# Performance work log

Hardware: AMD Instinct MI355X
Metric: run time of the kernel (lower is better)

Reference implementation:

```python
import jax, jax.numpy as jnp
import numpy as np

DIM = 512; NH = 8; AG = 144; WIN = 18; PS = 12; B = 128; N0 = 320


def _pool_matrix(in_size, out_size):
    # PyTorch AdaptiveAvgPool2d window rule: start=floor(i*in/out), end=ceil((i+1)*in/out)
    P = np.zeros((out_size, in_size), np.float32)
    for i in range(out_size):
        s = (i * in_size) // out_size
        e = -((-(i + 1) * in_size) // out_size)
        P[i, s:e] = 1.0 / (e - s)
    return jnp.asarray(P)


def setup_inputs() -> dict:
    key = jax.random.key(0)
    ks = jax.random.split(key, 12)
    std = 0.02
    return {
        "x": jax.random.normal(ks[0], (B, N0, DIM), jnp.float32),
        "qkv_w": jax.random.normal(ks[1], (DIM, 3 * DIM), jnp.float32) * 0.02,
        "proj_w": jax.random.normal(ks[2], (DIM, DIM), jnp.float32) * 0.02,
        "proj_b": jnp.zeros((DIM,), jnp.float32),
        "dwc_w": jax.random.normal(ks[3], (DIM, 1, 3, 3), jnp.float32) * 0.1,
        "dwc_b": jnp.zeros((DIM,), jnp.float32),
        "an_bias": jax.random.normal(ks[4], (NH, AG, 7, 7), jnp.float32) * std,
        "na_bias": jax.random.normal(ks[5], (NH, AG, 7, 7), jnp.float32) * std,
        "ah_bias": jax.random.normal(ks[6], (1, NH, AG, WIN, 1), jnp.float32) * std,
        "aw_bias": jax.random.normal(ks[7], (1, NH, AG, 1, WIN), jnp.float32) * std,
        "ha_bias": jax.random.normal(ks[8], (1, NH, WIN, 1, AG), jnp.float32) * std,
        "wa_bias": jax.random.normal(ks[9], (1, NH, 1, WIN, AG), jnp.float32) * std,
    }


def reference(x, qkv_w, proj_w, proj_b, dwc_w, dwc_b,
              an_bias, na_bias, ah_bias, aw_bias, ha_bias, wa_bias):
    b, n0, c = x.shape
    x1 = jnp.pad(x, ((0, 0), (2, 2), (0, 0)))          # pad 2 tokens each side
    n = n0 + 4
    h = w = int(n ** 0.5)
    hd = c // NH
    scale = hd ** -0.5

    qkv = x1 @ qkv_w                                    # (b, n, 3c), no bias
    q, k, v = jnp.split(qkv, 3, axis=-1)

    # agent tokens: adaptive avg pool of q on the (h, w) grid to (PS, PS)
    P = _pool_matrix(h, PS)                             # (12, 18)
    qg = q.reshape(b, h, w, c)
    agent = jnp.einsum('oh,bhwc,pw->bopc', P, qg, P).reshape(b, AG, c)

    def heads(t):
        return t.reshape(b, n, NH, hd).transpose(0, 2, 1, 3)
    q, k, v = heads(q), heads(k), heads(v)              # (b, H, n, hd)
    ag = agent.reshape(b, AG, NH, hd).transpose(0, 2, 1, 3)  # (b, H, A, hd)

    # stage 1: agent <- keys  (ac_bias is concatenated then sliced off => no-op)
    pb1 = jax.image.resize(an_bias, (NH, AG, WIN, WIN), 'bilinear').reshape(1, NH, AG, WIN * WIN)
    pb2 = (ah_bias + aw_bias).reshape(1, NH, AG, WIN * WIN)
    agent_attn = jax.nn.softmax(
        jnp.einsum('bhad,bhnd->bhan', ag * scale, k) + pb1 + pb2, axis=-1)
    agent_v = jnp.einsum('bhan,bhnd->bhad', agent_attn, v)   # (b, H, A, hd)

    # stage 2: queries <- agents (ca_bias sliced off => no-op)
    ab1 = jax.image.resize(na_bias, (NH, AG, WIN, WIN), 'bilinear') \
        .reshape(1, NH, AG, WIN * WIN).transpose(0, 1, 3, 2)  # (1, H, n, A)
    ab2 = (ha_bias + wa_bias).reshape(1, NH, WIN * WIN, AG)
    q_attn = jax.nn.softmax(
        jnp.einsum('bhnd,bhad->bhna', q * scale, ag) + ab1 + ab2, axis=-1)
    out = jnp.einsum('bhna,bhad->bhnd', q_attn, agent_v)
    out = out.transpose(0, 2, 1, 3).reshape(b, n, c)

    # depthwise conv skip on v
    vimg = v.transpose(0, 2, 1, 3).reshape(b, h, w, c).transpose(0, 3, 1, 2)  # (b, c, h, w)
    dwc = jax.lax.conv_general_dilated(vimg, dwc_w, (1, 1), 'SAME',
                                       feature_group_count=c)
    dwc = dwc + dwc_b[None, :, None, None]
    out = out + dwc.transpose(0, 2, 3, 1).reshape(b, n, c)

    out = out @ proj_w + proj_b
    return out[:, 2:-2, :]
```

## Files before the change

### kernel.cpp

```cpp
#include <hip/hip_runtime.h>

typedef unsigned short u16;
typedef short bf16x8 __attribute__((ext_vector_type(8)));
typedef float f32x4 __attribute__((ext_vector_type(4)));

#define B_    128
#define N0_   320
#define C_    512
#define NH_   8
#define HD_   64
#define NTOK  324
#define H_    18
#define AG_   144
#define SCALE 0.125f

typedef __attribute__((address_space(3))) unsigned int as3_u32;
typedef __attribute__((address_space(1))) const unsigned int as1_u32;

__device__ __forceinline__ void gl_lds16(const void* g, void* l) {
  __builtin_amdgcn_global_load_lds((as1_u32*)(unsigned long long)g,
                                   (as3_u32*)(unsigned int)(unsigned long long)l,
                                   16, 0, 0);
}

__device__ __forceinline__ float bfu2f(u16 u) {
  union { unsigned int u; float f; } v; v.u = ((unsigned int)u) << 16; return v.f;
}
__device__ __forceinline__ u16 f2bfu(float f) {
  union { float f; unsigned int u; } v; v.f = f;
  unsigned int r = v.u + 0x7fffu + ((v.u >> 16) & 1u);
  return (u16)(r >> 16);
}

__global__ __launch_bounds__(256) void conv_x(const float* __restrict__ x, u16* __restrict__ xp)
{
  const int idx = blockIdx.x * 256 + threadIdx.x;
  const int row = idx >> 6, c8 = idx & 63;
  const int b = row / NTOK, t = row - b * NTOK;
  u16 o[8];
  if (t < 2 || t >= 322) {
    #pragma unroll
    for (int j = 0; j < 8; ++j) o[j] = 0;
  } else {
    const float* src = x + ((size_t)(b * N0_ + (t - 2))) * C_ + c8 * 8;
    const float4 f0 = *(const float4*)(src);
    const float4 f1 = *(const float4*)(src + 4);
    o[0]=f2bfu(f0.x); o[1]=f2bfu(f0.y); o[2]=f2bfu(f0.z); o[3]=f2bfu(f0.w);
    o[4]=f2bfu(f1.x); o[5]=f2bfu(f1.y); o[6]=f2bfu(f1.z); o[7]=f2bfu(f1.w);
  }
  *(bf16x8*)&xp[(size_t)row * C_ + c8 * 8] = *(bf16x8*)o;
}

__global__ __launch_bounds__(256) void tconv(const float* __restrict__ W, u16* __restrict__ Wt, int ncols)
{
  __shared__ float T[64][65];
  const int k0 = blockIdx.x * 64, n0 = blockIdx.y * 64;
  const int tid = threadIdx.x;
  const int rr = tid >> 4, cc = tid & 15;
  #pragma unroll
  for (int i = 0; i < 4; ++i) {
    const float4 f = *(const float4*)&W[(size_t)(k0 + i * 16 + rr) * ncols + n0 + cc * 4];
    T[i * 16 + rr][cc * 4 + 0] = f.x; T[i * 16 + rr][cc * 4 + 1] = f.y;
    T[i * 16 + rr][cc * 4 + 2] = f.z; T[i * 16 + rr][cc * 4 + 3] = f.w;
  }
  __syncthreads();
  #pragma unroll
  for (int i = 0; i < 4; ++i) {
    const int n = i * 16 + rr;
    ushort4 u;
    u.x = f2bfu(T[cc * 4 + 0][n]); u.y = f2bfu(T[cc * 4 + 1][n]);
    u.z = f2bfu(T[cc * 4 + 2][n]); u.w = f2bfu(T[cc * 4 + 3][n]);
    *(ushort4*)&Wt[(size_t)(n0 + n) * 512 + k0 + cc * 4] = u;
  }
}

template<int MODE>
__global__ __launch_bounds__(256) void mfma_gemm(
    const u16* __restrict__ A, const u16* __restrict__ Bt,
    u16* __restrict__ qb, u16* __restrict__ kb, u16* __restrict__ vb,
    const float* __restrict__ bias, float* __restrict__ outf)
{
  __shared__ __align__(16) u16 As[128 * 64];
  __shared__ __align__(16) u16 Bs[128 * 64];
  const int bx = blockIdx.x;
  const int by = blockIdx.y;
  const int tid = threadIdx.x;
  const int wv = tid >> 6, lane = tid & 63;
  const int lr = lane & 15, lk = lane >> 4;
  const int wr = wv >> 1, wc = wv & 1;
  const int si = lane >> 3, slot = lane & 7;

  size_t arow_src[4];
  #pragma unroll
  for (int jj = 0; jj < 4; ++jj) {
    const int rl = (wv * 4 + jj) * 8 + si;
    const int r = by * 128 + rl;
    if (MODE == 0) {
      arow_src[jj] = (size_t)r * 512;
    } else {
      const int b2 = r / N0_, ii = r - b2 * N0_;
      arow_src[jj] = ((size_t)b2 * 8 * NTOK + (ii + 2)) * 64;
    }
  }

  f32x4 acc[4][4] = {};
  for (int k0 = 0; k0 < 512; k0 += 64) {
    __syncthreads();
    #pragma unroll
    for (int jj = 0; jj < 4; ++jj) {
      const int rl = (wv * 4 + jj) * 8 + si;
      const int c = slot ^ (rl & 7);
      const u16* asrc = (MODE == 0)
          ? (A + arow_src[jj] + k0 + c * 8)
          : (A + arow_src[jj] + (size_t)(k0 >> 6) * (NTOK * 64) + c * 8);
      gl_lds16(asrc, (char*)As + (wv * 4 + jj) * 1024);
      gl_lds16(Bt + (size_t)(bx * 128 + rl) * 512 + k0 + c * 8,
               (char*)Bs + (wv * 4 + jj) * 1024);
    }
    __syncthreads();
    #pragma unroll
    for (int kk = 0; kk < 2; ++kk) {
      bf16x8 af[4], bf[4];
      #pragma unroll
      for (int m = 0; m < 4; ++m) {
        const int row = wr * 64 + m * 16 + lr;
        af[m] = *(const bf16x8*)((const char*)As + row * 128 + (((kk * 4 + lk) ^ (row & 7)) << 4));
      }
      #pragma unroll
      for (int n = 0; n < 4; ++n) {
        const int row = wc * 64 + n * 16 + lr;
        bf[n] = *(const bf16x8*)((const char*)Bs + row * 128 + (((kk * 4 + lk) ^ (row & 7)) << 4));
      }
      #pragma unroll
      for (int m = 0; m < 4; ++m)
        #pragma unroll
        for (int n = 0; n < 4; ++n)
          acc[m][n] = __builtin_amdgcn_mfma_f32_16x16x32_bf16(bf[n], af[m], acc[m][n], 0, 0, 0);
    }
  }

  if (MODE == 0) {
    const int mat = (bx * 128) >> 9;
    u16* outp = (mat == 0) ? qb : (mat == 1) ? kb : vb;
    #pragma unroll
    for (int m = 0; m < 4; ++m) {
      const int row = by * 128 + wr * 64 + m * 16 + lr;
      const int b = row / NTOK, t = row - b * NTOK;
      #pragma unroll
      for (int n = 0; n < 4; ++n) {
        const int col = bx * 128 + wc * 64 + n * 16 + lk * 4;
        const int rem = col & 511, h = rem >> 6, d = rem & 63;
        ushort4 u;
        u.x = f2bfu(acc[m][n][0]); u.y = f2bfu(acc[m][n][1]);
        u.z = f2bfu(acc[m][n][2]); u.w = f2bfu(acc[m][n][3]);
        *(ushort4*)&outp[(((size_t)(b * NH_ + h)) * NTOK + t) * HD_ + d] = u;
      }
    }
  } else {
    #pragma unroll
    for (int m = 0; m < 4; ++m) {
      const int row = by * 128 + wr * 64 + m * 16 + lr;
      #pragma unroll
      for (int n = 0; n < 4; ++n) {
        const int col = bx * 128 + wc * 64 + n * 16 + lk * 4;
        float4 o;
        o.x = acc[m][n][0] + bias[col + 0];
        o.y = acc[m][n][1] + bias[col + 1];
        o.z = acc[m][n][2] + bias[col + 2];
        o.w = acc[m][n][3] + bias[col + 3];
        *(float4*)&outf[(size_t)row * C_ + col] = o;
      }
    }
  }
}

__global__ void bias_kernel(const float* __restrict__ an, const float* __restrict__ na,
                            const float* __restrict__ ah, const float* __restrict__ aw,
                            const float* __restrict__ ha, const float* __restrict__ wa,
                            u16* __restrict__ bANT, u16* __restrict__ bNAT)
{
  const int blk = blockIdx.x;
  const int h = blk / AG_, a = blk - h * AG_;
  const int tid = threadIdx.x;
  if (tid >= NTOK) return;
  const int y = tid / H_, x = tid - y * H_;
  float cy = (y + 0.5f) * (7.0f / 18.0f) - 0.5f; cy = fminf(fmaxf(cy, 0.f), 6.f);
  float cx = (x + 0.5f) * (7.0f / 18.0f) - 0.5f; cx = fminf(fmaxf(cx, 0.f), 6.f);
  const int y0 = (int)floorf(cy); const float ty = cy - y0; const int y1 = min(y0 + 1, 6);
  const int x0 = (int)floorf(cx); const float tx = cx - x0; const int x1 = min(x0 + 1, 6);
  const float w00 = (1.f - ty) * (1.f - tx), w01 = (1.f - ty) * tx;
  const float w10 = ty * (1.f - tx), w11 = ty * tx;
  const float* anp = an + (size_t)blk * 49;
  const float* nap = na + (size_t)blk * 49;
  const float van = w00 * anp[y0*7+x0] + w01 * anp[y0*7+x1] + w10 * anp[y1*7+x0] + w11 * anp[y1*7+x1];
  const float vna = w00 * nap[y0*7+x0] + w01 * nap[y0*7+x1] + w10 * nap[y1*7+x0] + w11 * nap[y1*7+x1];
  bANT[((size_t)h * NTOK + tid) * AG_ + a] =
      f2bfu(van + ah[(size_t)blk * H_ + y] + aw[(size_t)blk * H_ + x]);
  bNAT[((size_t)h * AG_ + a) * NTOK + tid] =
      f2bfu(vna + ha[((size_t)h * H_ + y) * AG_ + a] + wa[((size_t)h * H_ + x) * AG_ + a]);
}

__global__ __launch_bounds__(512) void pool_kernel(const u16* __restrict__ qb, u16* __restrict__ agb)
{
  const int blk = blockIdx.x;
  const int b = blk / AG_, a = blk - b * AG_;
  const int o = a / 12, pc = a - o * 12;
  const int y0 = (3 * o) >> 1, x0 = (3 * pc) >> 1;
  const int c = threadIdx.x; const int h = c >> 6, d = c & 63;
  const size_t base = ((size_t)(b * NH_ + h)) * NTOK * HD_ + d;
  const int t00 = (y0 * H_ + x0) * HD_;
  const float v = bfu2f(qb[base + t00]) + bfu2f(qb[base + t00 + HD_])
                + bfu2f(qb[base + t00 + H_ * HD_]) + bfu2f(qb[base + t00 + H_ * HD_ + HD_]);
  agb[((size_t)(b * NH_ + h)) * AG_ * HD_ + a * HD_ + d] = f2bfu(0.25f * v);
}

__global__ __launch_bounds__(512) void dwc_kernel(
    const u16* __restrict__ vb, const float* __restrict__ dwc_w,
    const float* __restrict__ dwc_b, u16* __restrict__ aob)
{
  __shared__ __align__(16) u16 vL[NTOK * 64];
  const int hb = blockIdx.x, h = hb >> 7, b = hb & 127;
  const int bh = b * NH_ + h;
  const int tid = threadIdx.x;
  const bf16x8* vs = (const bf16x8*)(vb + (size_t)bh * NTOK * HD_);
  for (int idx = tid; idx < NTOK * 8; idx += 512)
    ((bf16x8*)vL)[idx] = vs[idx];
  const int d = tid & 63, tg = tid >> 6;
  float w9[9];
  #pragma unroll
  for (int j = 0; j < 9; ++j) w9[j] = dwc_w[(size_t)(h * 64 + d) * 9 + j];
  const float cb = dwc_b[h * 64 + d];
  __syncthreads();
  u16* aout = aob + (size_t)bh * NTOK * HD_;
  for (int t = tg; t < NTOK; t += 8) {
    const int y = t / H_, x = t - y * H_;
    float conv = cb;
    #pragma unroll
    for (int ky = 0; ky < 3; ++ky) {
      const int yy = y + ky - 1;
      if (yy < 0 || yy >= H_) continue;
      #pragma unroll
      for (int kx = 0; kx < 3; ++kx) {
        const int xc = x + kx - 1;
        if (xc < 0 || xc >= H_) continue;
        conv += w9[ky * 3 + kx] * bfu2f(vL[(yy * H_ + xc) * 64 + d]);
      }
    }
    aout[(size_t)t * HD_ + d] = f2bfu(conv);
  }
}

__global__ __launch_bounds__(576) void stage1_k(
    const u16* __restrict__ kb, const u16* __restrict__ vb,
    const u16* __restrict__ agb, const u16* __restrict__ bANT,
    u16* __restrict__ avbT)
{
  __shared__ __align__(16) u16 vT[64 * 360];
  __shared__ __align__(16) u16 pW[9][16][40];
  const int hb = blockIdx.x, h = hb & 7, bbase = (hb >> 3) * 2;
  const int tid = threadIdx.x;
  const int mt = tid >> 6, l = tid & 63, lr = l & 15, lk = l >> 4;

  for (int bb2 = 0; bb2 < 2; ++bb2) {
    const int bh = (bbase + bb2) * NH_ + h;

    const u16* vsrc = vb + (size_t)bh * NTOK * HD_;
    for (int idx = tid; idx < 64 * 45; idx += 576) {
      const int d = idx & 63, c = idx >> 6;
      bf16x8 tv;
      #pragma unroll
      for (int j = 0; j < 8; ++j) {
        const int n = c * 8 + j;
        tv[j] = (n < NTOK) ? (short)vsrc[(size_t)n * HD_ + d] : (short)0;
      }
      *(bf16x8*)&vT[d * 360 + c * 8] = tv;
    }

    const u16* aga = agb + ((size_t)bh * AG_ + mt * 16 + lr) * HD_ + lk * 8;
    const bf16x8 a0 = *(const bf16x8*)(aga);
    const bf16x8 a1 = *(const bf16x8*)(aga + 32);

    f32x4 acc[21];
    const u16* kbase = kb + (size_t)bh * NTOK * HD_ + lk * 8;
    __builtin_amdgcn_s_setprio(1);
    #pragma unroll
    for (int nt = 0; nt < 21; ++nt) {
      const bf16x8 b0 = *(const bf16x8*)(kbase + (size_t)(nt * 16 + lr) * HD_);
      const bf16x8 b1 = *(const bf16x8*)(kbase + (size_t)(nt * 16 + lr) * HD_ + 32);
      f32x4 c = {0.f, 0.f, 0.f, 0.f};
      c = __builtin_amdgcn_mfma_f32_16x16x32_bf16(a0, b0, c, 0, 0, 0);
      c = __builtin_amdgcn_mfma_f32_16x16x32_bf16(a1, b1, c, 0, 0, 0);
      acc[nt] = c;
    }
    __builtin_amdgcn_s_setprio(0);

    float mx[4] = {-1e30f, -1e30f, -1e30f, -1e30f};
    #pragma unroll
    for (int nt = 0; nt < 21; ++nt) {
      const int t = nt * 16 + lr;
      const bool valid = (nt < 20) || (lr < 4);
      ushort4 b4 = make_ushort4(0, 0, 0, 0);
      if (valid)
        b4 = *(const ushort4*)&bANT[((size_t)h * NTOK + t) * AG_ + mt * 16 + lk * 4];
      #pragma unroll
      for (int r = 0; r < 4; ++r) {
        float s = -1e30f;
        if (valid) s = acc[nt][r] * SCALE + bfu2f(((const u16*)&b4)[r]);
        acc[nt][r] = s;
        mx[r] = fmaxf(mx[r], s);
      }
    }
    #pragma unroll
    for (int r = 0; r < 4; ++r) {
      #pragma unroll
      for (int o = 1; o < 16; o <<= 1) mx[r] = fmaxf(mx[r], __shfl_xor(mx[r], o));
    }
    float sm[4] = {0.f, 0.f, 0.f, 0.f};
    #pragma unroll
    for (int nt = 0; nt < 21; ++nt) {
      #pragma unroll
      for (int r = 0; r < 4; ++r) {
        const float e = __expf(acc[nt][r] - mx[r]);
        acc[nt][r] = e;
        sm[r] += e;
      }
    }
    #pragma unroll
    for (int r = 0; r < 4; ++r) {
      #pragma unroll
      for (int o = 1; o < 16; o <<= 1) sm[r] += __shfl_xor(sm[r], o);
      sm[r] = 1.0f / sm[r];
    }

    __syncthreads();

    f32x4 ov[4];
    #pragma unroll
    for (int nt2 = 0; nt2 < 4; ++nt2) ov[nt2] = (f32x4){0.f, 0.f, 0.f, 0.f};
    for (int ks = 0; ks < 11; ++ks) {
      #pragma unroll
      for (int half = 0; half < 2; ++half) {
        const int nt = 2 * ks + half;
        #pragma unroll
        for (int r = 0; r < 4; ++r)
          pW[mt][lk * 4 + r][half * 16 + lr] = (nt < 21) ? f2bfu(acc[nt][r] * sm[r]) : (u16)0;
      }
      const bf16x8 pa = *(const bf16x8*)&pW[mt][lr][lk * 8];
      __builtin_amdgcn_s_setprio(1);
      #pragma unroll
      for (int nt2 = 0; nt2 < 4; ++nt2) {
        const bf16x8 vf = *(const bf16x8*)&vT[(nt2 * 16 + lr) * 360 + ks * 32 + lk * 8];
        ov[nt2] = __builtin_amdgcn_mfma_f32_16x16x32_bf16(pa, vf, ov[nt2], 0, 0, 0);
      }
      __builtin_amdgcn_s_setprio(0);
    }

    __syncthreads();

    u16* avTL = vT;
    #pragma unroll
    for (int nt2 = 0; nt2 < 4; ++nt2) {
      ushort4 u;
      u.x = f2bfu(ov[nt2][0]); u.y = f2bfu(ov[nt2][1]);
      u.z = f2bfu(ov[nt2][2]); u.w = f2bfu(ov[nt2][3]);
      *(ushort4*)&avTL[(nt2 * 16 + lr) * 168 + mt * 16 + lk * 4] = u;
    }
    for (int idx = tid; idx < 128; idx += 576)
      *(bf16x8*)&avTL[(idx >> 1) * 168 + 144 + (idx & 1) * 8] = (bf16x8){0,0,0,0,0,0,0,0};

    __syncthreads();

    u16* dst = avbT + (size_t)bh * 64 * 160;
    for (int idx = tid; idx < 64 * 20; idx += 576) {
      const int d = idx / 20, c = idx - d * 20;
      *(bf16x8*)&dst[d * 160 + c * 8] = *(const bf16x8*)&avTL[d * 168 + c * 8];
    }
    __syncthreads();
  }
}

__global__ __launch_bounds__(512, 6) void stage2_k(
    const u16* __restrict__ qb, const u16* __restrict__ agb,
    const u16* __restrict__ avbT, const u16* __restrict__ bNAT,
    u16* __restrict__ aob)
{
  __shared__ __align__(16) u16 avT[64 * 168];
  __shared__ __align__(16) u16 pW[8][16][40];
  __shared__ __align__(16) u16 oB[8][16][72];
  const int hb = blockIdx.x, h = hb & 7, bbase = (hb >> 3) * 2;
  const int tid = threadIdx.x;
  const int wv = tid >> 6, l = tid & 63, lr = l & 15, lk = l >> 4;

  for (int bb2 = 0; bb2 < 2; ++bb2) {
    const int bh = (bbase + bb2) * NH_ + h;

    const u16* src = avbT + (size_t)bh * 64 * 160;
    for (int idx = tid; idx < 64 * 20; idx += 512) {
      const int d = idx / 20, c = idx - d * 20;
      *(bf16x8*)&avT[d * 168 + c * 8] = *(const bf16x8*)&src[d * 160 + c * 8];
    }
    __syncthreads();

    u16* aout = aob + (size_t)bh * NTOK * HD_;
    for (int mt2 = wv; mt2 < 21; mt2 += 8) {
      const int arow = min(mt2 * 16 + lr, NTOK - 1);
      const u16* qa = qb + ((size_t)bh * NTOK + arow) * HD_ + lk * 8;
      const bf16x8 qa0 = *(const bf16x8*)(qa);
      const bf16x8 qa1 = *(const bf16x8*)(qa + 32);

      f32x4 acc2[9];
      __builtin_amdgcn_s_setprio(1);
      #pragma unroll
      for (int nt = 0; nt < 9; ++nt) {
        const u16* bp = agb + ((size_t)bh * AG_ + nt * 16 + lr) * HD_ + lk * 8;
        f32x4 c = {0.f, 0.f, 0.f, 0.f};
        c = __builtin_amdgcn_mfma_f32_16x16x32_bf16(qa0, *(const bf16x8*)(bp), c, 0, 0, 0);
        c = __builtin_amdgcn_mfma_f32_16x16x32_bf16(qa1, *(const bf16x8*)(bp + 32), c, 0, 0, 0);
        acc2[nt] = c;
      }
      __builtin_amdgcn_s_setprio(0);

      float mx2[4] = {-1e30f, -1e30f, -1e30f, -1e30f};
      const int t0 = mt2 * 16 + lk * 4;
      #pragma unroll
      for (int nt = 0; nt < 9; ++nt) {
        const ushort4 b4 = *(const ushort4*)&bNAT[((size_t)h * AG_ + nt * 16 + lr) * NTOK + t0];
        #pragma unroll
        for (int r = 0; r < 4; ++r) {
          const float s = acc2[nt][r] * SCALE + bfu2f(((const u16*)&b4)[r]);
          acc2[nt][r] = s;
          mx2[r] = fmaxf(mx2[r], s);
        }
      }
      #pragma unroll
      for (int r = 0; r < 4; ++r) {
        #pragma unroll
        for (int o = 1; o < 16; o <<= 1) mx2[r] = fmaxf(mx2[r], __shfl_xor(mx2[r], o));
      }
      float sm2[4] = {0.f, 0.f, 0.f, 0.f};
      #pragma unroll
      for (int nt = 0; nt < 9; ++nt) {
        #pragma unroll
        for (int r = 0; r < 4; ++r) {
          const float e = __expf(acc2[nt][r] - mx2[r]);
          acc2[nt][r] = e;
          sm2[r] += e;
        }
      }
      #pragma unroll
      for (int r = 0; r < 4; ++r) {
        #pragma unroll
        for (int o = 1; o < 16; o <<= 1) sm2[r] += __shfl_xor(sm2[r], o);
        sm2[r] = 1.0f / sm2[r];
      }

      f32x4 ov2[4];
      #pragma unroll
      for (int dt = 0; dt < 4; ++dt) ov2[dt] = (f32x4){0.f, 0.f, 0.f, 0.f};
      for (int ks = 0; ks < 5; ++ks) {
        #pragma unroll
        for (int half = 0; half < 2; ++half) {
          const int nt = 2 * ks + half;
          #pragma unroll
          for (int r = 0; r < 4; ++r)
            pW[wv][lk * 4 + r][half * 16 + lr] = (nt < 9) ? f2bfu(acc2[nt][r] * sm2[r]) : (u16)0;
        }
        const bf16x8 pa = *(const bf16x8*)&pW[wv][lr][lk * 8];
        __builtin_amdgcn_s_setprio(1);
        #pragma unroll
        for (int dt = 0; dt < 4; ++dt) {
          const bf16x8 vf = *(const bf16x8*)&avT[(dt * 16 + lr) * 168 + ks * 32 + lk * 8];
          ov2[dt] = __builtin_amdgcn_mfma_f32_16x16x32_bf16(vf, pa, ov2[dt], 0, 0, 0);
        }
        __builtin_amdgcn_s_setprio(0);
      }

      #pragma unroll
      for (int dt = 0; dt < 4; ++dt) {
        ushort4 u;
        u.x = f2bfu(ov2[dt][0]); u.y = f2bfu(ov2[dt][1]);
        u.z = f2bfu(ov2[dt][2]); u.w = f2bfu(ov2[dt][3]);
        *(ushort4*)&oB[wv][lr][dt * 16 + lk * 4] = u;
      }
      const int tloc = l >> 2, part = l & 3;
      if (mt2 * 16 + tloc < NTOK) {
        u16* gp = &aout[(size_t)(mt2 * 16 + tloc) * HD_ + part * 16];
        const u16* lp = &oB[wv][tloc][part * 16];
        const bf16x8 g0 = *(const bf16x8*)(gp);
        const bf16x8 g1 = *(const bf16x8*)(gp + 8);
        const bf16x8 l0 = *(const bf16x8*)(lp);
        const bf16x8 l1 = *(const bf16x8*)(lp + 8);
        bf16x8 o0, o1;
        #pragma unroll
        for (int j = 0; j < 8; ++j) {
          o0[j] = (short)f2bfu(bfu2f((u16)g0[j]) + bfu2f((u16)l0[j]));
          o1[j] = (short)f2bfu(bfu2f((u16)g1[j]) + bfu2f((u16)l1[j]));
        }
        *(bf16x8*)(gp) = o0;
        *(bf16x8*)(gp + 8) = o1;
      }
    }
    __syncthreads();
  }
}

extern "C" void kernel_launch(void* const* d_in, const int* in_sizes, int n_in,
                              void* d_out, int out_size, void* d_ws, size_t ws_size,
                              hipStream_t stream)
{
  (void)in_sizes; (void)n_in; (void)out_size;
  const float* x      = (const float*)d_in[0];
  const float* qkv_w  = (const float*)d_in[1];
  const float* proj_w = (const float*)d_in[2];
  const float* proj_b = (const float*)d_in[3];
  const float* dwc_w  = (const float*)d_in[4];
  const float* dwc_b  = (const float*)d_in[5];
  const float* an     = (const float*)d_in[6];
  const float* na     = (const float*)d_in[7];
  const float* ah     = (const float*)d_in[8];
  const float* aw     = (const float*)d_in[9];
  const float* ha     = (const float*)d_in[10];
  const float* wa     = (const float*)d_in[11];

  char* ws = (char*)d_ws;
  const size_t QB   = (size_t)B_ * NH_ * NTOK * HD_ * 2;
  const size_t AGB  = (size_t)B_ * NH_ * AG_  * HD_ * 2;
  const size_t AVTB = (size_t)B_ * NH_ * 64 * 160 * 2;
  const size_t BB   = (size_t)NH_ * AG_ * NTOK * 2 + 64;
  const size_t WQ   = (size_t)1536 * 512 * 2;
  const size_t WP   = (size_t)512 * 512 * 2;
  u16* qb    = (u16*)(ws);
  u16* kb    = (u16*)(ws + QB);
  u16* vb    = (u16*)(ws + 2 * QB);
  u16* xp    = (u16*)(ws + 3 * QB);
  u16* agb   = (u16*)(ws + 3 * QB);
  u16* avbT  = (u16*)(ws + 3 * QB + AGB);
  u16* bANT  = (u16*)(ws + 3 * QB + AGB + AVTB);
  u16* wqkvT = (u16*)(ws + 4 * QB);
  u16* wprojT= (u16*)(ws + 4 * QB + WQ);
  u16* bNAT  = (u16*)(ws + 4 * QB + WQ + WP);
  u16* aob   = kb;
  if (ws_size < 4 * QB + WQ + WP + BB) return;

  conv_x   <<<dim3(B_ * NTOK * 64 / 256), dim3(256), 0, stream>>>(x, xp);
  tconv    <<<dim3(8, 24), dim3(256), 0, stream>>>(qkv_w, wqkvT, 1536);
  tconv    <<<dim3(8, 8),  dim3(256), 0, stream>>>(proj_w, wprojT, 512);
  mfma_gemm<0><<<dim3(12, 324), dim3(256), 0, stream>>>(xp, wqkvT, qb, kb, vb, nullptr, nullptr);
  pool_kernel<<<dim3(B_ * AG_),  dim3(512), 0, stream>>>(qb, agb);
  bias_kernel<<<dim3(NH_ * AG_), dim3(324), 0, stream>>>(an, na, ah, aw, ha, wa, bANT, bNAT);
  stage1_k <<<dim3(NH_ * B_ / 2), dim3(576), 0, stream>>>(kb, vb, agb, bANT, avbT);
  dwc_kernel<<<dim3(NH_ * B_), dim3(512), 0, stream>>>(vb, dwc_w, dwc_b, aob);
  stage2_k <<<dim3(NH_ * B_ / 2), dim3(512), 0, stream>>>(qb, agb, avbT, bNAT, aob);
  mfma_gemm<1><<<dim3(4, 320), dim3(256), 0, stream>>>(aob, wprojT, nullptr, nullptr, nullptr, proj_b, (float*)d_out);
}
```

Measured before the change: 531.0 us.

## Fuse depthwise conv into stage1 and process one batch-head per block

```diff
diff --git a/kernel.cpp b/kernel.cpp
--- a/kernel.cpp
+++ b/kernel.cpp
@@ -214,293 +214,276 @@
   agb[((size_t)(b * NH_ + h)) * AG_ * HD_ + a * HD_ + d] = f2bfu(0.25f * v);
 }
 
-__global__ __launch_bounds__(512) void dwc_kernel(
-    const u16* __restrict__ vb, const float* __restrict__ dwc_w,
-    const float* __restrict__ dwc_b, u16* __restrict__ aob)
-{
-  __shared__ __align__(16) u16 vL[NTOK * 64];
-  const int hb = blockIdx.x, h = hb >> 7, b = hb & 127;
-  const int bh = b * NH_ + h;
-  const int tid = threadIdx.x;
-  const bf16x8* vs = (const bf16x8*)(vb + (size_t)bh * NTOK * HD_);
-  for (int idx = tid; idx < NTOK * 8; idx += 512)
-    ((bf16x8*)vL)[idx] = vs[idx];
-  const int d = tid & 63, tg = tid >> 6;
-  float w9[9];
-  #pragma unroll
-  for (int j = 0; j < 9; ++j) w9[j] = dwc_w[(size_t)(h * 64 + d) * 9 + j];
-  const float cb = dwc_b[h * 64 + d];
-  __syncthreads();
-  u16* aout = aob + (size_t)bh * NTOK * HD_;
-  for (int t = tg; t < NTOK; t += 8) {
-    const int y = t / H_, x = t - y * H_;
-    float conv = cb;
-    #pragma unroll
-    for (int ky = 0; ky < 3; ++ky) {
-      const int yy = y + ky - 1;
-      if (yy < 0 || yy >= H_) continue;
-      #pragma unroll
-      for (int kx = 0; kx < 3; ++kx) {
-        const int xc = x + kx - 1;
-        if (xc < 0 || xc >= H_) continue;
-        conv += w9[ky * 3 + kx] * bfu2f(vL[(yy * H_ + xc) * 64 + d]);
-      }
-    }
-    aout[(size_t)t * HD_ + d] = f2bfu(conv);
-  }
-}
-
 __global__ __launch_bounds__(576) void stage1_k(
     const u16* __restrict__ kb, const u16* __restrict__ vb,
     const u16* __restrict__ agb, const u16* __restrict__ bANT,
-    u16* __restrict__ avbT)
+    const float* __restrict__ dwc_w, const float* __restrict__ dwc_b,
+    u16* __restrict__ avbT, u16* __restrict__ aob)
 {
   __shared__ __align__(16) u16 vT[64 * 360];
   __shared__ __align__(16) u16 pW[9][16][40];
-  const int hb = blockIdx.x, h = hb & 7, bbase = (hb >> 3) * 2;
+  const int hb = blockIdx.x, h = hb & 7, b = hb >> 3;
+  const int bh = b * NH_ + h;
   const int tid = threadIdx.x;
   const int mt = tid >> 6, l = tid & 63, lr = l & 15, lk = l >> 4;
 
-  for (int bb2 = 0; bb2 < 2; ++bb2) {
-    const int bh = (bbase + bb2) * NH_ + h;
-
-    const u16* vsrc = vb + (size_t)bh * NTOK * HD_;
-    for (int idx = tid; idx < 64 * 45; idx += 576) {
-      const int d = idx & 63, c = idx >> 6;
-      bf16x8 tv;
-      #pragma unroll
-      for (int j = 0; j < 8; ++j) {
-        const int n = c * 8 + j;
-        tv[j] = (n < NTOK) ? (short)vsrc[(size_t)n * HD_ + d] : (short)0;
-      }
-      *(bf16x8*)&vT[d * 360 + c * 8] = tv;
-    }
-
-    const u16* aga = agb + ((size_t)bh * AG_ + mt * 16 + lr) * HD_ + lk * 8;
-    const bf16x8 a0 = *(const bf16x8*)(aga);
-    const bf16x8 a1 = *(const bf16x8*)(aga + 32);
-
-    f32x4 acc[21];
-    const u16* kbase = kb + (size_t)bh * NTOK * HD_ + lk * 8;
+  const u16* vsrc = vb + (size_t)bh * NTOK * HD_;
+  for (int idx = tid; idx < 64 * 45; idx += 576) {
+    const int d = idx & 63, c = idx >> 6;
+    bf16x8 tv;
+    #pragma unroll
+    for (int j = 0; j < 8; ++j) {
+      const int n = c * 8 + j;
+      tv[j] = (n < NTOK) ? (short)vsrc[(size_t)n * HD_ + d] : (short)0;
+    }
+    *(bf16x8*)&vT[d * 360 + c * 8] = tv;
+  }
+
+  const u16* aga = agb + ((size_t)bh * AG_ + mt * 16 + lr) * HD_ + lk * 8;
+  const bf16x8 a0 = *(const bf16x8*)(aga);
+  const bf16x8 a1 = *(const bf16x8*)(aga + 32);
+
+  f32x4 acc[21];
+  const u16* kbase = kb + (size_t)bh * NTOK * HD_ + lk * 8;
+  __builtin_amdgcn_s_setprio(1);
+  #pragma unroll
+  for (int nt = 0; nt < 21; ++nt) {
+    const bf16x8 b0 = *(const bf16x8*)(kbase + (size_t)(nt * 16 + lr) * HD_);
+    const bf16x8 b1 = *(const bf16x8*)(kbase + (size_t)(nt * 16 + lr) * HD_ + 32);
+    f32x4 c = {0.f, 0.f, 0.f, 0.f};
+    c = __builtin_amdgcn_mfma_f32_16x16x32_bf16(a0, b0, c, 0, 0, 0);
+    c = __builtin_amdgcn_mfma_f32_16x16x32_bf16(a1, b1, c, 0, 0, 0);
+    acc[nt] = c;
+  }
+  __builtin_amdgcn_s_setprio(0);
+
+  float mx[4] = {-1e30f, -1e30f, -1e30f, -1e30f};
+  #pragma unroll
+  for (int nt = 0; nt < 21; ++nt) {
+    const int t = nt * 16 + lr;
+    const bool valid = (nt < 20) || (lr < 4);
+    ushort4 b4 = make_ushort4(0, 0, 0, 0);
+    if (valid)
+      b4 = *(const ushort4*)&bANT[((size_t)h * NTOK + t) * AG_ + mt * 16 + lk * 4];
+    #pragma unroll
+    for (int r = 0; r < 4; ++r) {
+      float s = -1e30f;
+      if (valid) s = acc[nt][r] * SCALE + bfu2f(((const u16*)&b4)[r]);
+      acc[nt][r] = s;
+      mx[r] = fmaxf(mx[r], s);
+    }
+  }
+  #pragma unroll
+  for (int r = 0; r < 4; ++r) {
+    #pragma unroll
+    for (int o = 1; o < 16; o <<= 1) mx[r] = fmaxf(mx[r], __shfl_xor(mx[r], o));
+  }
+  float sm[4] = {0.f, 0.f, 0.f, 0.f};
+  #pragma unroll
+  for (int nt = 0; nt < 21; ++nt) {
+    #pragma unroll
+    for (int r = 0; r < 4; ++r) {
+      const float e = __expf(acc[nt][r] - mx[r]);
+      acc[nt][r] = e;
+      sm[r] += e;
+    }
+  }
+  #pragma unroll
+  for (int r = 0; r < 4; ++r) {
+    #pragma unroll
+    for (int o = 1; o < 16; o <<= 1) sm[r] += __shfl_xor(sm[r], o);
+    sm[r] = 1.0f / sm[r];
+  }
+
+  __syncthreads();
+
+  f32x4 ov[4];
+  #pragma unroll
+  for (int nt2 = 0; nt2 < 4; ++nt2) ov[nt2] = (f32x4){0.f, 0.f, 0.f, 0.f};
+  for (int ks = 0; ks < 11; ++ks) {
+    #pragma unroll
+    for (int half = 0; half < 2; ++half) {
+      const int nt = 2 * ks + half;
+      #pragma unroll
+      for (int r = 0; r < 4; ++r)
+        pW[mt][lk * 4 + r][half * 16 + lr] = (nt < 21) ? f2bfu(acc[nt][r] * sm[r]) : (u16)0;
+    }
+    const bf16x8 pa = *(const bf16x8*)&pW[mt][lr][lk * 8];
     __builtin_amdgcn_s_setprio(1);
     #pragma unroll
-    for (int nt = 0; nt < 21; ++nt) {
-      const bf16x8 b0 = *(const bf16x8*)(kbase + (size_t)(nt * 16 + lr) * HD_);
-      const bf16x8 b1 = *(const bf16x8*)(kbase + (size_t)(nt * 16 + lr) * HD_ + 32);
+    for (int nt2 = 0; nt2 < 4; ++nt2) {
+      const bf16x8 vf = *(const bf16x8*)&vT[(nt2 * 16 + lr) * 360 + ks * 32 + lk * 8];
+      ov[nt2] = __builtin_amdgcn_mfma_f32_16x16x32_bf16(pa, vf, ov[nt2], 0, 0, 0);
+    }
+    __builtin_amdgcn_s_setprio(0);
+  }
+
+  {
+    const int d = l;
+    float w9[9];
+    #pragma unroll
+    for (int j = 0; j < 9; ++j) w9[j] = dwc_w[(size_t)(h * 64 + d) * 9 + j];
+    const float cb = dwc_b[h * 64 + d];
+    u16* aout = aob + (size_t)bh * NTOK * HD_;
+    for (int i = 0; i < 36; ++i) {
+      const int t = mt * 36 + i;
+      const int y = t / H_, x = t - y * H_;
+      float conv = cb;
+      #pragma unroll
+      for (int ky = 0; ky < 3; ++ky) {
+        const int yy = y + ky - 1;
+        if (yy < 0 || yy >= H_) continue;
+        #pragma unroll
+        for (int kx = 0; kx < 3; ++kx) {
+          const int xc = x + kx - 1;
+          if (xc < 0 || xc >= H_) continue;
+          conv += w9[ky * 3 + kx] * bfu2f(vT[d * 360 + yy * H_ + xc]);
+        }
+      }
+      aout[(size_t)t * HD_ + d] = f2bfu(conv);
+    }
+  }
+
+  __syncthreads();
+
+  u16* avTL = vT;
+  #pragma unroll
+  for (int nt2 = 0; nt2 < 4; ++nt2) {
+    ushort4 u;
+    u.x = f2bfu(ov[nt2][0]); u.y = f2bfu(ov[nt2][1]);
+    u.z = f2bfu(ov[nt2][2]); u.w = f2bfu(ov[nt2][3]);
+    *(ushort4*)&avTL[(nt2 * 16 + lr) * 168 + mt * 16 + lk * 4] = u;
+  }
+  for (int idx = tid; idx < 128; idx += 576)
+    *(bf16x8*)&avTL[(idx >> 1) * 168 + 144 + (idx & 1) * 8] = (bf16x8){0,0,0,0,0,0,0,0};
+
+  __syncthreads();
+
+  u16* dst = avbT + (size_t)bh * 64 * 160;
+  for (int idx = tid; idx < 64 * 20; idx += 576) {
+    const int d = idx / 20, c = idx - d * 20;
+    *(bf16x8*)&dst[d * 160 + c * 8] = *(const bf16x8*)&avTL[d * 168 + c * 8];
+  }
+}
+
+__global__ __launch_bounds__(512, 6) void stage2_k(
+    const u16* __restrict__ qb, const u16* __restrict__ agb,
+    const u16* __restrict__ avbT, const u16* __restrict__ bNAT,
+    u16* __restrict__ aob)
+{
+  __shared__ __align__(16) u16 avT[64 * 168];
+  __shared__ __align__(16) u16 pW[8][16][40];
+  __shared__ __align__(16) u16 oB[8][16][72];
+  const int hb = blockIdx.x, h = hb & 7, b = hb >> 3;
+  const int bh = b * NH_ + h;
+  const int tid = threadIdx.x;
+  const int wv = tid >> 6, l = tid & 63, lr = l & 15, lk = l >> 4;
+
+  const u16* src = avbT + (size_t)bh * 64 * 160;
+  for (int idx = tid; idx < 64 * 20; idx += 512) {
+    const int d = idx / 20, c = idx - d * 20;
+    *(bf16x8*)&avT[d * 168 + c * 8] = *(const bf16x8*)&src[d * 160 + c * 8];
+  }
+  __syncthreads();
+
+  u16* aout = aob + (size_t)bh * NTOK * HD_;
+  for (int mt2 = wv; mt2 < 21; mt2 += 8) {
+    const int arow = min(mt2 * 16 + lr, NTOK - 1);
+    const u16* qa = qb + ((size_t)bh * NTOK + arow) * HD_ + lk * 8;
+    const bf16x8 qa0 = *(const bf16x8*)(qa);
+    const bf16x8 qa1 = *(const bf16x8*)(qa + 32);
+
+    f32x4 acc2[9];
+    __builtin_amdgcn_s_setprio(1);
+    #pragma unroll
+    for (int nt = 0; nt < 9; ++nt) {
+      const u16* bp = agb + ((size_t)bh * AG_ + nt * 16 + lr) * HD_ + lk * 8;
       f32x4 c = {0.f, 0.f, 0.f, 0.f};
-      c = __builtin_amdgcn_mfma_f32_16x16x32_bf16(a0, b0, c, 0, 0, 0);
-      c = __builtin_amdgcn_mfma_f32_16x16x32_bf16(a1, b1, c, 0, 0, 0);
-      acc[nt] = c;
+      c = __builtin_amdgcn_mfma_f32_16x16x32_bf16(qa0, *(const bf16x8*)(bp), c, 0, 0, 0);
+      c = __builtin_amdgcn_mfma_f32_16x16x32_bf16(qa1, *(const bf16x8*)(bp + 32), c, 0, 0, 0);
+      acc2[nt] = c;
     }
     __builtin_amdgcn_s_setprio(0);
 
-    float mx[4] = {-1e30f, -1e30f, -1e30f, -1e30f};
-    #pragma unroll
-    for (int nt = 0; nt < 21; ++nt) {
-      const int t = nt * 16 + lr;
-      const bool valid = (nt < 20) || (lr < 4);
-      ushort4 b4 = make_ushort4(0, 0, 0, 0);
-      if (valid)
-        b4 = *(const ushort4*)&bANT[((size_t)h * NTOK + t) * AG_ + mt * 16 + lk * 4];
+    float mx2[4] = {-1e30f, -1e30f, -1e30f, -1e30f};
+    const int t0 = mt2 * 16 + lk * 4;
+    #pragma unroll
+    for (int nt = 0; nt < 9; ++nt) {
+      const ushort4 b4 = *(const ushort4*)&bNAT[((size_t)h * AG_ + nt * 16 + lr) * NTOK + t0];
       #pragma unroll
       for (int r = 0; r < 4; ++r) {
-        float s = -1e30f;
-        if (valid) s = acc[nt][r] * SCALE + bfu2f(((const u16*)&b4)[r]);
-        acc[nt][r] = s;
-        mx[r] = fmaxf(mx[r], s);
+        const float s = acc2[nt][r] * SCALE + bfu2f(((const u16*)&b4)[r]);
+        acc2[nt][r] = s;
+        mx2[r] = fmaxf(mx2[r], s);
       }
     }
     #pragma unroll
     for (int r = 0; r < 4; ++r) {
       #pragma unroll
-      for (int o = 1; o < 16; o <<= 1) mx[r] = fmaxf(mx[r], __shfl_xor(mx[r], o));
-    }
-    float sm[4] = {0.f, 0.f, 0.f, 0.f};
-    #pragma unroll
-    for (int nt = 0; nt < 21; ++nt) {
+      for (int o = 1; o < 16; o <<= 1) mx2[r] = fmaxf(mx2[r], __shfl_xor(mx2[r], o));
+    }
+    float sm2[4] = {0.f, 0.f, 0.f, 0.f};
+    #pragma unroll
+    for (int nt = 0; nt < 9; ++nt) {
       #pragma unroll
       for (int r = 0; r < 4; ++r) {
-        const float e = __expf(acc[nt][r] - mx[r]);
-        acc[nt][r] = e;
-        sm[r] += e;
+        const float e = __expf(acc2[nt][r] - mx2[r]);
+        acc2[nt][r] = e;
+        sm2[r] += e;
       }
     }
     #pragma unroll
     for (int r = 0; r < 4; ++r) {
       #pragma unroll
-      for (int o = 1; o < 16; o <<= 1) sm[r] += __shfl_xor(sm[r], o);
-      sm[r] = 1.0f / sm[r];
-    }
-
-    __syncthreads();
-
-    f32x4 ov[4];
-    #pragma unroll
-    for (int nt2 = 0; nt2 < 4; ++nt2) ov[nt2] = (f32x4){0.f, 0.f, 0.f, 0.f};
-    for (int ks = 0; ks < 11; ++ks) {
+      for (int o = 1; o < 16; o <<= 1) sm2[r] += __shfl_xor(sm2[r], o);
+      sm2[r] = 1.0f / sm2[r];
+    }
+
+    f32x4 ov2[4];
+    #pragma unroll
+    for (int dt = 0; dt < 4; ++dt) ov2[dt] = (f32x4){0.f, 0.f, 0.f, 0.f};
+    for (int ks = 0; ks < 5; ++ks) {
       #pragma unroll
       for (int half = 0; half < 2; ++half) {
         const int nt = 2 * ks + half;
         #pragma unroll
         for (int r = 0; r < 4; ++r)
-          pW[mt][lk * 4 + r][half * 16 + lr] = (nt < 21) ? f2bfu(acc[nt][r] * sm[r]) : (u16)0;
-      }
-      const bf16x8 pa = *(const bf16x8*)&pW[mt][lr][lk * 8];
+          pW[wv][lk * 4 + r][half * 16 + lr] = (nt < 9) ? f2bfu(acc2[nt][r] * sm2[r]) : (u16)0;
+      }
+      const bf16x8 pa = *(const bf16x8*)&pW[wv][lr][lk * 8];
       __builtin_amdgcn_s_setprio(1);
       #pragma unroll
-      for (int nt2 = 0; nt2 < 4; ++nt2) {
-        const bf16x8 vf = *(const bf16x8*)&vT[(nt2 * 16 + lr) * 360 + ks * 32 + lk * 8];
-        ov[nt2] = __builtin_amdgcn_mfma_f32_16x16x32_bf16(pa, vf, ov[nt2], 0, 0, 0);
+      for (int dt = 0; dt < 4; ++dt) {
+        const bf16x8 vf = *(const bf16x8*)&avT[(dt * 16 + lr) * 168 + ks * 32 + lk * 8];
+        ov2[dt] = __builtin_amdgcn_mfma_f32_16x16x32_bf16(vf, pa, ov2[dt], 0, 0, 0);
       }
       __builtin_amdgcn_s_setprio(0);
     }
 
-    __syncthreads();
-
-    u16* avTL = vT;
-    #pragma unroll
-    for (int nt2 = 0; nt2 < 4; ++nt2) {
+    #pragma unroll
+    for (int dt = 0; dt < 4; ++dt) {
       ushort4 u;
-      u.x = f2bfu(ov[nt2][0]); u.y = f2bfu(ov[nt2][1]);
-      u.z = f2bfu(ov[nt2][2]); u.w = f2bfu(ov[nt2][3]);
-      *(ushort4*)&avTL[(nt2 * 16 + lr) * 168 + mt * 16 + lk * 4] = u;
-    }
-    for (int idx = tid; idx < 128; idx += 576)
-      *(bf16x8*)&avTL[(idx >> 1) * 168 + 144 + (idx & 1) * 8] = (bf16x8){0,0,0,0,0,0,0,0};
-
-    __syncthreads();
-
-    u16* dst = avbT + (size_t)bh * 64 * 160;
-    for (int idx = tid; idx < 64 * 20; idx += 576) {
-      const int d = idx / 20, c = idx - d * 20;
-      *(bf16x8*)&dst[d * 160 + c * 8] = *(const bf16x8*)&avTL[d * 168 + c * 8];
-    }
-    __syncthreads();
-  }
-}
-
-__global__ __launch_bounds__(512, 6) void stage2_k(
-    const u16* __restrict__ qb, const u16* __restrict__ agb,
-    const u16* __restrict__ avbT, const u16* __restrict__ bNAT,
-    u16* __restrict__ aob)
-{
-  __shared__ __align__(16) u16 avT[64 * 168];
-  __shared__ __align__(16) u16 pW[8][16][40];
-  __shared__ __align__(16) u16 oB[8][16][72];
-  const int hb = blockIdx.x, h = hb & 7, bbase = (hb >> 3) * 2;
-  const int tid = threadIdx.x;
-  const int wv = tid >> 6, l = tid & 63, lr = l & 15, lk = l >> 4;
-
-  for (int bb2 = 0; bb2 < 2; ++bb2) {
-    const int bh = (bbase + bb2) * NH_ + h;
-
-    const u16* src = avbT + (size_t)bh * 64 * 160;
-    for (int idx = tid; idx < 64 * 20; idx += 512) {
-      const int d = idx / 20, c = idx - d * 20;
-      *(bf16x8*)&avT[d * 168 + c * 8] = *(const bf16x8*)&src[d * 160 + c * 8];
-    }
-    __syncthreads();
-
-    u16* aout = aob + (size_t)bh * NTOK * HD_;
-    for (int mt2 = wv; mt2 < 21; mt2 += 8) {
-      const int arow = min(mt2 * 16 + lr, NTOK - 1);
-      const u16* qa = qb + ((size_t)bh * NTOK + arow) * HD_ + lk * 8;
-      const bf16x8 qa0 = *(const bf16x8*)(qa);
-      const bf16x8 qa1 = *(const bf16x8*)(qa + 32);
-
-      f32x4 acc2[9];
-      __builtin_amdgcn_s_setprio(1);
-      #pragma unroll
-      for (int nt = 0; nt < 9; ++nt) {
-        const u16* bp = agb + ((size_t)bh * AG_ + nt * 16 + lr) * HD_ + lk * 8;
-        f32x4 c = {0.f, 0.f, 0.f, 0.f};
-        c = __builtin_amdgcn_mfma_f32_16x16x32_bf16(qa0, *(const bf16x8*)(bp), c, 0, 0, 0);
-        c = __builtin_amdgcn_mfma_f32_16x16x32_bf16(qa1, *(const bf16x8*)(bp + 32), c, 0, 0, 0);
-        acc2[nt] = c;
-      }
-      __builtin_amdgcn_s_setprio(0);
-
-      float mx2[4] = {-1e30f, -1e30f, -1e30f, -1e30f};
-      const int t0 = mt2 * 16 + lk * 4;
-      #pragma unroll
-      for (int nt = 0; nt < 9; ++nt) {
-        const ushort4 b4 = *(const ushort4*)&bNAT[((size_t)h * AG_ + nt * 16 + lr) * NTOK + t0];
-        #pragma unroll
-        for (int r = 0; r < 4; ++r) {
-          const float s = acc2[nt][r] * SCALE + bfu2f(((const u16*)&b4)[r]);
-          acc2[nt][r] = s;
-          mx2[r] = fmaxf(mx2[r], s);
-        }
-      }
-      #pragma unroll
-      for (int r = 0; r < 4; ++r) {
-        #pragma unroll
-        for (int o = 1; o < 16; o <<= 1) mx2[r] = fmaxf(mx2[r], __shfl_xor(mx2[r], o));
-      }
-      float sm2[4] = {0.f, 0.f, 0.f, 0.f};
-      #pragma unroll
-      for (int nt = 0; nt < 9; ++nt) {
-        #pragma unroll
-        for (int r = 0; r < 4; ++r) {
-          const float e = __expf(acc2[nt][r] - mx2[r]);
-          acc2[nt][r] = e;
-          sm2[r] += e;
-        }
-      }
-      #pragma unroll
-      for (int r = 0; r < 4; ++r) {
-        #pragma unroll
-        for (int o = 1; o < 16; o <<= 1) sm2[r] += __shfl_xor(sm2[r], o);
-        sm2[r] = 1.0f / sm2[r];
-      }
-
-      f32x4 ov2[4];
-      #pragma unroll
-      for (int dt = 0; dt < 4; ++dt) ov2[dt] = (f32x4){0.f, 0.f, 0.f, 0.f};
-      for (int ks = 0; ks < 5; ++ks) {
-        #pragma unroll
-        for (int half = 0; half < 2; ++half) {
-          const int nt = 2 * ks + half;
-          #pragma unroll
-          for (int r = 0; r < 4; ++r)
-            pW[wv][lk * 4 + r][half * 16 + lr] = (nt < 9) ? f2bfu(acc2[nt][r] * sm2[r]) : (u16)0;
-        }
-        const bf16x8 pa = *(const bf16x8*)&pW[wv][lr][lk * 8];
-        __builtin_amdgcn_s_setprio(1);
-        #pragma unroll
-        for (int dt = 0; dt < 4; ++dt) {
-          const bf16x8 vf = *(const bf16x8*)&avT[(dt * 16 + lr) * 168 + ks * 32 + lk * 8];
-          ov2[dt] = __builtin_amdgcn_mfma_f32_16x16x32_bf16(vf, pa, ov2[dt], 0, 0, 0);
-        }
-        __builtin_amdgcn_s_setprio(0);
-      }
-
-      #pragma unroll
-      for (int dt = 0; dt < 4; ++dt) {
-        ushort4 u;
-        u.x = f2bfu(ov2[dt][0]); u.y = f2bfu(ov2[dt][1]);
-        u.z = f2bfu(ov2[dt][2]); u.w = f2bfu(ov2[dt][3]);
-        *(ushort4*)&oB[wv][lr][dt * 16 + lk * 4] = u;
-      }
-      const int tloc = l >> 2, part = l & 3;
-      if (mt2 * 16 + tloc < NTOK) {
-        u16* gp = &aout[(size_t)(mt2 * 16 + tloc) * HD_ + part * 16];
-        const u16* lp = &oB[wv][tloc][part * 16];
-        const bf16x8 g0 = *(const bf16x8*)(gp);
-        const bf16x8 g1 = *(const bf16x8*)(gp + 8);
-        const bf16x8 l0 = *(const bf16x8*)(lp);
-        const bf16x8 l1 = *(const bf16x8*)(lp + 8);
-        bf16x8 o0, o1;
-        #pragma unroll
-        for (int j = 0; j < 8; ++j) {
-          o0[j] = (short)f2bfu(bfu2f((u16)g0[j]) + bfu2f((u16)l0[j]));
-          o1[j] = (short)f2bfu(bfu2f((u16)g1[j]) + bfu2f((u16)l1[j]));
-        }
-        *(bf16x8*)(gp) = o0;
-        *(bf16x8*)(gp + 8) = o1;
-      }
-    }
-    __syncthreads();
+      u.x = f2bfu(ov2[dt][0]); u.y = f2bfu(ov2[dt][1]);
+      u.z = f2bfu(ov2[dt][2]); u.w = f2bfu(ov2[dt][3]);
+      *(ushort4*)&oB[wv][lr][dt * 16 + lk * 4] = u;
+    }
+    const int tloc = l >> 2, part = l & 3;
+    if (mt2 * 16 + tloc < NTOK) {
+      u16* gp = &aout[(size_t)(mt2 * 16 + tloc) * HD_ + part * 16];
+      const u16* lp = &oB[wv][tloc][part * 16];
+      const bf16x8 g0 = *(const bf16x8*)(gp);
+      const bf16x8 g1 = *(const bf16x8*)(gp + 8);
+      const bf16x8 l0 = *(const bf16x8*)(lp);
+      const bf16x8 l1 = *(const bf16x8*)(lp + 8);
+      bf16x8 o0, o1;
+      #pragma unroll
+      for (int j = 0; j < 8; ++j) {
+        o0[j] = (short)f2bfu(bfu2f((u16)g0[j]) + bfu2f((u16)l0[j]));
+        o1[j] = (short)f2bfu(bfu2f((u16)g1[j]) + bfu2f((u16)l1[j]));
+      }
+      *(bf16x8*)(gp) = o0;
+      *(bf16x8*)(gp + 8) = o1;
+    }
   }
 }
 
@@ -548,8 +531,7 @@
   mfma_gemm<0><<<dim3(12, 324), dim3(256), 0, stream>>>(xp, wqkvT, qb, kb, vb, nullptr, nullptr);
   pool_kernel<<<dim3(B_ * AG_),  dim3(512), 0, stream>>>(qb, agb);
   bias_kernel<<<dim3(NH_ * AG_), dim3(324), 0, stream>>>(an, na, ah, aw, ha, wa, bANT, bNAT);
-  stage1_k <<<dim3(NH_ * B_ / 2), dim3(576), 0, stream>>>(kb, vb, agb, bANT, avbT);
-  dwc_kernel<<<dim3(NH_ * B_), dim3(512), 0, stream>>>(vb, dwc_w, dwc_b, aob);
-  stage2_k <<<dim3(NH_ * B_ / 2), dim3(512), 0, stream>>>(qb, agb, avbT, bNAT, aob);
+  stage1_k <<<dim3(NH_ * B_), dim3(576), 0, stream>>>(kb, vb, agb, bANT, dwc_w, dwc_b, avbT, aob);
+  stage2_k <<<dim3(NH_ * B_), dim3(512), 0, stream>>>(qb, agb, avbT, bNAT, aob);
   mfma_gemm<1><<<dim3(4, 320), dim3(256), 0, stream>>>(aob, wprojT, nullptr, nullptr, nullptr, proj_b, (float*)d_out);
 }
```

After: 524.1 us. No clear change (-1.3%).
